# Optimization experiments

Hardware: AMD Instinct MI355X
Metric: run time of the kernel (lower is better)

The kernel has to match this reference:

```python
import jax, jax.numpy as jnp
import numpy as np

LB = 8      # luma bins
CM = 1      # channel multiplier
GC = 16     # guide complexity
NIN, NOUT = 4, 3
BN_EPS = 1e-5


def bilateral_slice(grid, guide):
    # grid: [B, gh, gw, gd, C]; guide: [B, H, W] in [0,1]
    B, gh, gw, gd, C = grid.shape
    _, H, W = guide.shape
    dt = guide.dtype
    hg = (jnp.arange(H, dtype=dt) + 0.5) * (gh / H) - 0.5   # [H]
    wg = (jnp.arange(W, dtype=dt) + 0.5) * (gw / W) - 0.5   # [W]
    zg = guide * gd - 0.5                                    # [B,H,W]
    h0 = jnp.floor(hg); w0 = jnp.floor(wg); z0 = jnp.floor(zg)
    fh = hg - h0; fw = wg - w0; fz = zg - z0
    h0 = h0.astype(jnp.int32); w0 = w0.astype(jnp.int32); z0 = z0.astype(jnp.int32)
    bidx = jnp.arange(B)[:, None, None]
    out = jnp.zeros((B, H, W, C), dtype=grid.dtype)
    for dh in (0, 1):
        hi = jnp.clip(h0 + dh, 0, gh - 1)          # [H]
        wh_h = fh if dh else (1.0 - fh)
        for dw in (0, 1):
            wi = jnp.clip(w0 + dw, 0, gw - 1)      # [W]
            wh_w = fw if dw else (1.0 - fw)
            w_hw = (wh_h[:, None] * wh_w[None, :])[None]  # [1,H,W]
            for dz in (0, 1):
                zi = jnp.clip(z0 + dz, 0, gd - 1)  # [B,H,W]
                wh_z = fz if dz else (1.0 - fz)
                g = grid[bidx, hi[None, :, None], wi[None, None, :], zi]  # [B,H,W,C]
                out = out + g * (w_hw * wh_z)[..., None]
    return out


def conv1x1(x, w, b):
    # x: [B,Cin,H,W], w: [Cout,Cin], b: [Cout]
    return jnp.einsum('oc,bchw->bohw', w, x) + b[None, :, None, None]


def setup_inputs() -> dict:
    key = jax.random.key(0)
    ks = jax.random.split(key, 12)
    B, H, W, GH, GW = 4, 1024, 1024, 16, 16
    fullres = jax.random.uniform(ks[0], (B, 3, H, W), dtype=jnp.float32)
    local_features = jax.random.normal(ks[1], (B, 8 * CM * LB, GH, GW), dtype=jnp.float32)
    global_features = jax.random.normal(ks[2], (B, 8 * CM * LB), dtype=jnp.float32)
    cout = LB * NOUT * NIN  # 96
    fusion_w = jax.random.normal(ks[3], (cout, 8 * CM * LB), dtype=jnp.float32) * 0.1
    fusion_b = jnp.zeros((cout,), dtype=jnp.float32)
    g1_w = jax.random.normal(ks[4], (GC, 3), dtype=jnp.float32) * 0.5
    g1_b = jnp.zeros((GC,), dtype=jnp.float32)
    bn_gamma = jnp.ones((GC,), dtype=jnp.float32)
    bn_beta = jnp.zeros((GC,), dtype=jnp.float32)
    bn_mean = jnp.zeros((GC,), dtype=jnp.float32)
    bn_var = jnp.ones((GC,), dtype=jnp.float32)
    g2_w = jax.random.normal(ks[5], (1, GC), dtype=jnp.float32) * 0.3
    g2_b = jnp.zeros((1,), dtype=jnp.float32)
    return dict(fullres=fullres, local_features=local_features, global_features=global_features,
                fusion_w=fusion_w, fusion_b=fusion_b, g1_w=g1_w, g1_b=g1_b,
                bn_gamma=bn_gamma, bn_beta=bn_beta, bn_mean=bn_mean, bn_var=bn_var,
                g2_w=g2_w, g2_b=g2_b)


def reference(fullres, local_features, global_features, fusion_w, fusion_b,
              g1_w, g1_b, bn_gamma, bn_beta, bn_mean, bn_var, g2_w, g2_b):
    B = fullres.shape[0]
    # Fusion: relu(local + broadcast global), then 1x1 conv to 96 channels
    fused = jax.nn.relu(local_features + global_features[:, :, None, None])
    x = conv1x1(fused, fusion_w, fusion_b)                    # [B,96,GH,GW]
    GH, GW = x.shape[2], x.shape[3]
    # split(12, dim=1) + stack(dim=2) -> [B,12,LB,GH,GW]
    coeffs = x.reshape(B, LB, NIN * NOUT, GH, GW).transpose(0, 2, 1, 3, 4)
    # GuideNN: 1x1 conv + BN(eval) + relu, then 1x1 conv + sigmoid
    g = conv1x1(fullres, g1_w, g1_b)
    g = (g - bn_mean[None, :, None, None]) * (bn_gamma[None, :, None, None] *
        jax.lax.rsqrt(bn_var + BN_EPS)[None, :, None, None]) + bn_beta[None, :, None, None]
    g = jax.nn.relu(g)
    guide = jax.nn.sigmoid(conv1x1(g, g2_w, g2_b))[:, 0]      # [B,H,W]
    # Slicing: permute grid to [B,GH,GW,LB,12], trilinear slice, back to NCHW
    grid = coeffs.transpose(0, 3, 4, 2, 1)
    sliced = bilateral_slice(grid, guide)                     # [B,H,W,12]
    coeff = sliced.transpose(0, 3, 1, 2)                      # [B,12,H,W]
    # ApplyCoeffs
    R = jnp.sum(fullres * coeff[:, 0:3], axis=1, keepdims=True) + coeff[:, 9:10]
    G = jnp.sum(fullres * coeff[:, 3:6], axis=1, keepdims=True) + coeff[:, 10:11]
    Bc = jnp.sum(fullres * coeff[:, 6:9], axis=1, keepdims=True) + coeff[:, 11:12]
    return jnp.tanh(jnp.concatenate([R, G, Bc], axis=1))
```

## Files before the change

### kernel.cpp

```cpp
#include <hip/hip_runtime.h>
#include <math.h>


#define GRIDBUF_FLOATS (4 * 16 * 16 * 96)

__device__ inline float fast_tanh(float x) {
    float ax = fabsf(x);
    float e  = __expf(2.0f * ax);
    float t  = 1.0f - 2.0f / (e + 1.0f);
    return copysignf(t, x);
}

__global__ __launch_bounds__(128) void coeff_kernel(
    const float* __restrict__ lf,
    const float* __restrict__ gf,
    const float* __restrict__ fw,
    const float* __restrict__ fb,
    const float* __restrict__ g1w,
    const float* __restrict__ g1b,
    const float* __restrict__ bng,
    const float* __restrict__ bnb,
    const float* __restrict__ bnm,
    const float* __restrict__ bnv,
    const float* __restrict__ g2w,
    const float* __restrict__ g2b,
    float* __restrict__ gridbuf,
    float* __restrict__ params)
{
    __shared__ float fused[64];
    const int blk = blockIdx.x;
    const int b   = blk >> 8;
    const int pos = blk & 255;
    const int t   = threadIdx.x;

    if (t < 64) {
        float v = lf[(b * 64 + t) * 256 + pos] + gf[b * 64 + t];
        fused[t] = v > 0.0f ? v : 0.0f;
    }
    __syncthreads();

    if (t < 96) {
        float acc = fb[t];
        const float* wrow = fw + t * 64;
#pragma unroll
        for (int i = 0; i < 64; ++i) acc = fmaf(wrow[i], fused[i], acc);
        gridbuf[blk * 96 + t] = acc;
    }

    if (blk == 0 && t >= 96 && t < 112) {
        int k = t - 96;
        float a = bng[k] * rsqrtf(bnv[k] + 1e-5f);
        params[k]      = g1w[k * 3 + 0] * a;
        params[16 + k] = g1w[k * 3 + 1] * a;
        params[32 + k] = g1w[k * 3 + 2] * a;
        params[48 + k] = (g1b[k] - bnm[k]) * a + bnb[k];
        params[64 + k] = g2w[k];
        if (k == 0) params[80] = g2b[0];
    }
}

__global__ __launch_bounds__(256) void slice_apply_kernel(
    const float* __restrict__ fullres,
    const float* __restrict__ gridbuf,
    const float* __restrict__ params,
    float* __restrict__ out)
{
    __shared__ __align__(16) float hrow[1536];
    __shared__ float P[81];

    const int t = threadIdx.x;
    const int b = blockIdx.x >> 10;
    const int y = blockIdx.x & 1023;

    if (t < 81) P[t] = params[t];

    float hg = (y + 0.5f) * 0.015625f - 0.5f;
    int   h0 = (int)floorf(hg);
    float fh = hg - (float)h0;
    int hc0 = h0 < 0 ? 0 : h0;
    int hc1 = (h0 + 1) > 15 ? 15 : (h0 + 1);

    const float* row0 = gridbuf + (b * 256 + hc0 * 16) * 96;
    const float* row1 = gridbuf + (b * 256 + hc1 * 16) * 96;
    const float wfh0 = 1.0f - fh;
#pragma unroll
    for (int i = t; i < 1536; i += 256)
        hrow[i] = fmaf(wfh0, row0[i], fh * row1[i]);
    __syncthreads();

    const int xb = t << 2;
    const int pixbase = (y << 10) + xb;
    const int planeB = (b * 3) << 20;

    const float4 r4 = *(const float4*)(fullres + planeB + (0 << 20) + pixbase);
    const float4 g4 = *(const float4*)(fullres + planeB + (1 << 20) + pixbase);
    const float4 b4 = *(const float4*)(fullres + planeB + (2 << 20) + pixbase);

    float oR[4], oG[4], oB[4];

#pragma unroll
    for (int j = 0; j < 4; ++j) {
        const float r  = (j == 0) ? r4.x : (j == 1) ? r4.y : (j == 2) ? r4.z : r4.w;
        const float g  = (j == 0) ? g4.x : (j == 1) ? g4.y : (j == 2) ? g4.z : g4.w;
        const float bl = (j == 0) ? b4.x : (j == 1) ? b4.y : (j == 2) ? b4.z : b4.w;

        float acc = P[80];
#pragma unroll
        for (int k = 0; k < 16; ++k) {
            float gk = fmaf(r, P[k], fmaf(g, P[16 + k], fmaf(bl, P[32 + k], P[48 + k])));
            gk = gk > 0.0f ? gk : 0.0f;
            acc = fmaf(gk, P[64 + k], acc);
        }
        const float guide = 1.0f / (1.0f + __expf(-acc));

        float wg = (float)(xb + j) * 0.015625f + (0.5f * 0.015625f - 0.5f);
        int   w0 = (int)floorf(wg);
        float fw_ = wg - (float)w0;
        int wc0 = w0 < 0 ? 0 : w0;
        int wc1 = (w0 + 1) > 15 ? 15 : (w0 + 1);

        float zg = fmaf(guide, 8.0f, -0.5f);
        int   z0 = (int)floorf(zg);
        float fz = zg - (float)z0;
        int zc0 = z0 < 0 ? 0 : z0;
        int zc1 = (z0 + 1) > 7 ? 7 : (z0 + 1);

        float s[12];
#pragma unroll
        for (int c = 0; c < 12; ++c) s[c] = 0.0f;

#pragma unroll
        for (int dw = 0; dw < 2; ++dw) {
            const int   wc  = dw ? wc1 : wc0;
            const float whw = dw ? fw_ : (1.0f - fw_);
            const float w0z = whw * (1.0f - fz);
            const float w1z = whw * fz;
            const float* cell = hrow + wc * 96;
            const float4* p0 = (const float4*)(cell + zc0 * 12);
            const float4* p1 = (const float4*)(cell + zc1 * 12);
#pragma unroll
            for (int q = 0; q < 3; ++q) {
                float4 a  = p0[q];
                float4 bq = p1[q];
                s[q * 4 + 0] = fmaf(w0z, a.x, fmaf(w1z, bq.x, s[q * 4 + 0]));
                s[q * 4 + 1] = fmaf(w0z, a.y, fmaf(w1z, bq.y, s[q * 4 + 1]));
                s[q * 4 + 2] = fmaf(w0z, a.z, fmaf(w1z, bq.z, s[q * 4 + 2]));
                s[q * 4 + 3] = fmaf(w0z, a.w, fmaf(w1z, bq.w, s[q * 4 + 3]));
            }
        }

        float Rv = fmaf(r, s[0], fmaf(g, s[1], fmaf(bl, s[2], s[9])));
        float Gv = fmaf(r, s[3], fmaf(g, s[4], fmaf(bl, s[5], s[10])));
        float Bv = fmaf(r, s[6], fmaf(g, s[7], fmaf(bl, s[8], s[11])));
        oR[j] = fast_tanh(Rv);
        oG[j] = fast_tanh(Gv);
        oB[j] = fast_tanh(Bv);
    }

    *(float4*)(out + planeB + (0 << 20) + pixbase) = make_float4(oR[0], oR[1], oR[2], oR[3]);
    *(float4*)(out + planeB + (1 << 20) + pixbase) = make_float4(oG[0], oG[1], oG[2], oG[3]);
    *(float4*)(out + planeB + (2 << 20) + pixbase) = make_float4(oB[0], oB[1], oB[2], oB[3]);
}

extern "C" void kernel_launch(void* const* d_in, const int* in_sizes, int n_in,
                              void* d_out, int out_size, void* d_ws, size_t ws_size,
                              hipStream_t stream) {
    const float* fullres = (const float*)d_in[0];
    const float* lf      = (const float*)d_in[1];
    const float* gf      = (const float*)d_in[2];
    const float* fw      = (const float*)d_in[3];
    const float* fb      = (const float*)d_in[4];
    const float* g1w     = (const float*)d_in[5];
    const float* g1b     = (const float*)d_in[6];
    const float* bng     = (const float*)d_in[7];
    const float* bnb     = (const float*)d_in[8];
    const float* bnm     = (const float*)d_in[9];
    const float* bnv     = (const float*)d_in[10];
    const float* g2w     = (const float*)d_in[11];
    const float* g2b     = (const float*)d_in[12];
    float* out = (float*)d_out;

    float* gridbuf = (float*)d_ws;
    float* params  = gridbuf + GRIDBUF_FLOATS;

    coeff_kernel<<<4 * 256, 128, 0, stream>>>(lf, gf, fw, fb, g1w, g1b,
                                              bng, bnb, bnm, bnv, g2w, g2b,
                                              gridbuf, params);
    slice_apply_kernel<<<4 * 1024, 256, 0, stream>>>(fullres, gridbuf, params, out);
}
```

Measured before the change: 149.4 us.

## Pad LDS cell stride, vectorize row blend, read params directly, nontemporal stores

Pads each grid cell in shared memory to a stride of 100 floats to reduce bank conflicts on the float4 trilinear gathers. The height blend is vectorized to float4. Guide parameters are read straight from global memory (uniform, scalar loads) instead of being staged in LDS. The w-index is computed with integer math, and outputs are written with nontemporal stores to avoid polluting cache. Risks are possible misaligned float4 accesses if the padding breaks 16-byte alignment (100*4 is 16-aligned, so it is fine) and extra scalar load traffic for the params.

Result: faster. 139.4 us (-6.7%).

```diff
diff --git a/kernel.cpp b/kernel.cpp
--- a/kernel.cpp
+++ b/kernel.cpp
@@ -3,6 +3,9 @@
 
 
 #define GRIDBUF_FLOATS (4 * 16 * 16 * 96)
+#define CELL_STRIDE 100
+
+typedef float vfloat4 __attribute__((ext_vector_type(4)));
 
 __device__ inline float fast_tanh(float x) {
     float ax = fabsf(x);
@@ -65,14 +68,11 @@
     const float* __restrict__ params,
     float* __restrict__ out)
 {
-    __shared__ __align__(16) float hrow[1536];
-    __shared__ float P[81];
+    __shared__ __align__(16) float hrow[16 * CELL_STRIDE];
 
     const int t = threadIdx.x;
     const int b = blockIdx.x >> 10;
     const int y = blockIdx.x & 1023;
-
-    if (t < 81) P[t] = params[t];
 
     float hg = (y + 0.5f) * 0.015625f - 0.5f;
     int   h0 = (int)floorf(hg);
@@ -84,8 +84,19 @@
     const float* row1 = gridbuf + (b * 256 + hc1 * 16) * 96;
     const float wfh0 = 1.0f - fh;
 #pragma unroll
-    for (int i = t; i < 1536; i += 256)
-        hrow[i] = fmaf(wfh0, row0[i], fh * row1[i]);
+    for (int i4 = t; i4 < 384; i4 += 256) {
+        const int i   = i4 << 2;
+        const int wc  = i / 96;
+        const int rem = i - wc * 96;
+        float4 a = *(const float4*)(row0 + i);
+        float4 c = *(const float4*)(row1 + i);
+        float4 r;
+        r.x = fmaf(wfh0, a.x, fh * c.x);
+        r.y = fmaf(wfh0, a.y, fh * c.y);
+        r.z = fmaf(wfh0, a.z, fh * c.z);
+        r.w = fmaf(wfh0, a.w, fh * c.w);
+        *(float4*)(hrow + wc * CELL_STRIDE + rem) = r;
+    }
     __syncthreads();
 
     const int xb = t << 2;
@@ -104,20 +115,22 @@
         const float g  = (j == 0) ? g4.x : (j == 1) ? g4.y : (j == 2) ? g4.z : g4.w;
         const float bl = (j == 0) ? b4.x : (j == 1) ? b4.y : (j == 2) ? b4.z : b4.w;
 
-        float acc = P[80];
+        float acc = params[80];
 #pragma unroll
         for (int k = 0; k < 16; ++k) {
-            float gk = fmaf(r, P[k], fmaf(g, P[16 + k], fmaf(bl, P[32 + k], P[48 + k])));
+            float gk = fmaf(r, params[k],
+                       fmaf(g, params[16 + k],
+                       fmaf(bl, params[32 + k], params[48 + k])));
             gk = gk > 0.0f ? gk : 0.0f;
-            acc = fmaf(gk, P[64 + k], acc);
+            acc = fmaf(gk, params[64 + k], acc);
         }
         const float guide = 1.0f / (1.0f + __expf(-acc));
 
-        float wg = (float)(xb + j) * 0.015625f + (0.5f * 0.015625f - 0.5f);
-        int   w0 = (int)floorf(wg);
-        float fw_ = wg - (float)w0;
-        int wc0 = w0 < 0 ? 0 : w0;
-        int wc1 = (w0 + 1) > 15 ? 15 : (w0 + 1);
+        const int x = xb + j;
+        const int w0i = (x < 32) ? -1 : ((x - 32) >> 6);
+        const float fw_ = ((float)x * 0.015625f + (0.0078125f - 0.5f)) - (float)w0i;
+        const int wc0 = w0i < 0 ? 0 : w0i;
+        const int wc1 = (w0i + 1) > 15 ? 15 : (w0i + 1);
 
         float zg = fmaf(guide, 8.0f, -0.5f);
         int   z0 = (int)floorf(zg);
@@ -135,7 +148,7 @@
             const float whw = dw ? fw_ : (1.0f - fw_);
             const float w0z = whw * (1.0f - fz);
             const float w1z = whw * fz;
-            const float* cell = hrow + wc * 96;
+            const float* cell = hrow + wc * CELL_STRIDE;
             const float4* p0 = (const float4*)(cell + zc0 * 12);
             const float4* p1 = (const float4*)(cell + zc1 * 12);
 #pragma unroll
@@ -157,9 +170,12 @@
         oB[j] = fast_tanh(Bv);
     }
 
-    *(float4*)(out + planeB + (0 << 20) + pixbase) = make_float4(oR[0], oR[1], oR[2], oR[3]);
-    *(float4*)(out + planeB + (1 << 20) + pixbase) = make_float4(oG[0], oG[1], oG[2], oG[3]);
-    *(float4*)(out + planeB + (2 << 20) + pixbase) = make_float4(oB[0], oB[1], oB[2], oB[3]);
+    vfloat4 vR = { oR[0], oR[1], oR[2], oR[3] };
+    vfloat4 vG = { oG[0], oG[1], oG[2], oG[3] };
+    vfloat4 vB = { oB[0], oB[1], oB[2], oB[3] };
+    __builtin_nontemporal_store(vR, (vfloat4*)(out + planeB + (0 << 20) + pixbase));
+    __builtin_nontemporal_store(vG, (vfloat4*)(out + planeB + (1 << 20) + pixbase));
+    __builtin_nontemporal_store(vB, (vfloat4*)(out + planeB + (2 << 20) + pixbase));
 }
 
 extern "C" void kernel_launch(void* const* d_in, const int* in_sizes, int n_in,
```
